# Optimization experiments

Hardware: AMD Instinct MI355X
Metric: run time of the kernel (lower is better)

The kernel has to match this reference:

```python
import jax, jax.numpy as jnp
import numpy as np

NCLASS = 19
BETA = 0.999
IGNORE = -1


def setup_inputs() -> dict:
    key = jax.random.key(0)
    k1, k2 = jax.random.split(key)
    logits = jax.random.normal(k1, (8, NCLASS, 512, 1024), dtype=jnp.float32)
    target = jax.random.randint(k2, (8, 512, 1024), 0, NCLASS, dtype=jnp.int32)
    return {"logits": logits, "target": target}


def _class_balanced_weights(target):
    # Vectorized replacement of the per-sample torch.histc loop.
    B = target.shape[0]
    t = target.reshape(B, -1)
    valid = (t >= 0) & (t < NCLASS)  # histc drops out-of-range (e.g. -1)
    seg = jnp.where(valid, jnp.arange(B, dtype=t.dtype)[:, None] * NCLASS + t, B * NCLASS)
    counts = jax.ops.segment_sum(
        jnp.ones(seg.size, dtype=jnp.float32), seg.reshape(-1),
        num_segments=B * NCLASS + 1)[: B * NCLASS].reshape(B, NCLASS)
    total = counts.sum(axis=0)  # [NCLASS] class counts over whole batch
    w = (1.0 - BETA) / (1.0 - jnp.power(jnp.float32(BETA), total))
    # torch code zeroes the inf entries (classes with zero count)
    return jnp.where(total > 0, w, 0.0)


def reference(logits, target):
    weights = _class_balanced_weights(target)  # [NCLASS]
    logp = jax.nn.log_softmax(logits, axis=1)  # [B, C, H, W]
    tc = jnp.clip(target, 0, NCLASS - 1)
    tgt_logp = jnp.take_along_axis(logp, tc[:, None].astype(jnp.int32), axis=1)[:, 0]  # [B, H, W]
    valid = (target != IGNORE).astype(logits.dtype)
    w_t = weights[tc] * valid  # per-pixel class weight, 0 at ignored pixels
    # PyTorch weighted cross_entropy 'mean': sum(w*nll) / sum(w) over valid
    loss = -(w_t * tgt_logp).sum() / w_t.sum()
    return loss
```

## Files before the change

kernel.cpp:

```cpp
#include <hip/hip_runtime.h>
#include <math.h>

#define NCLASS 19
#define IGNORE_LBL (-1)

constexpr int BDIM   = 8;
constexpr int HWDIM  = 512 * 1024;
constexpr int NPIX   = BDIM * HWDIM;
constexpr int NSTRIP = BDIM * NCLASS;
constexpr int PIXB   = 1024;
constexpr int RING   = 8;
constexpr int DEPTH  = 6;
constexpr double BETA = 0.999;

struct WS {
    double sums[NCLASS];
    int    counts[NCLASS];
};

__global__ void init_ws(WS* ws) {
    int t = threadIdx.x;
    if (t < NCLASS) { ws->sums[t] = 0.0; ws->counts[t] = 0; }
}

typedef const __attribute__((address_space(1))) void* as1_t;
typedef __attribute__((address_space(3))) void*       as3_t;

__device__ __forceinline__ void gload16(const float* g, float* l) {
    __builtin_amdgcn_global_load_lds((as1_t)g, (as3_t)l, 16, 0, 0);
}

__global__ __launch_bounds__(256)
void loss_fused_kernel(const float* __restrict__ logits, const int* __restrict__ tgt,
                       WS* __restrict__ ws) {
    __shared__ __align__(16) float ring[RING][PIXB];
    __shared__ float l_sum[NCLASS];
    __shared__ int   l_cnt[NCLASS];

    const int  tid = threadIdx.x;
    const int  wid = tid >> 6;
    const long px0 = (long)blockIdx.x * PIXB;

    if (tid < NCLASS) { l_sum[tid] = 0.f; l_cnt[tid] = 0; }
    __syncthreads();

    int4 t_cur = *reinterpret_cast<const int4*>(tgt + px0 + 4 * tid);

    const float* gissue = logits + px0 + wid * 256;
    const float* glast  = logits + px0 + (long)(NSTRIP - 1) * HWDIM + wid * 256;

#pragma unroll
    for (int s = 0; s < DEPTH; ++s) {
        gload16(gissue, &ring[s][wid * 256]);
        gissue += HWDIM;
    }

    int slot = 0;

#pragma unroll 1
    for (int b = 0; b < BDIM; ++b) {
        int4 t_nxt = t_cur;
        if (b + 1 < BDIM)
            t_nxt = *reinterpret_cast<const int4*>(
                tgt + (long)(b + 1) * HWDIM + px0 + 4 * tid);

        float s0 = 0.f, s1 = 0.f, s2 = 0.f, s3 = 0.f;
        float ta0 = 0.f, ta1 = 0.f, ta2 = 0.f, ta3 = 0.f;

#pragma unroll
        for (int c = 0; c < NCLASS; ++c) {
            gload16(gissue, &ring[(slot + DEPTH) & (RING - 1)][wid * 256]);
            if (gissue < glast) gissue += HWDIM;
            asm volatile("s_waitcnt vmcnt(6)" ::: "memory");
            __builtin_amdgcn_sched_barrier(0);

            float4 v = *reinterpret_cast<const float4*>(&ring[slot][4 * tid]);
            s0 += __expf(v.x);
            s1 += __expf(v.y);
            s2 += __expf(v.z);
            s3 += __expf(v.w);
            if (c == t_cur.x) ta0 = v.x;
            if (c == t_cur.y) ta1 = v.y;
            if (c == t_cur.z) ta2 = v.z;
            if (c == t_cur.w) ta3 = v.w;
            slot = (slot + 1) & (RING - 1);
        }

        if (t_cur.x >= 0 && t_cur.x < NCLASS) {
            atomicAdd(&l_sum[t_cur.x], ta0 - __logf(s0));
            atomicAdd(&l_cnt[t_cur.x], 1);
        }
        if (t_cur.y >= 0 && t_cur.y < NCLASS) {
            atomicAdd(&l_sum[t_cur.y], ta1 - __logf(s1));
            atomicAdd(&l_cnt[t_cur.y], 1);
        }
        if (t_cur.z >= 0 && t_cur.z < NCLASS) {
            atomicAdd(&l_sum[t_cur.z], ta2 - __logf(s2));
            atomicAdd(&l_cnt[t_cur.z], 1);
        }
        if (t_cur.w >= 0 && t_cur.w < NCLASS) {
            atomicAdd(&l_sum[t_cur.w], ta3 - __logf(s3));
            atomicAdd(&l_cnt[t_cur.w], 1);
        }

        t_cur = t_nxt;
    }

    __syncthreads();
    if (tid < NCLASS) {
        atomicAdd(&ws->sums[tid], (double)l_sum[tid]);
        atomicAdd(&ws->counts[tid], l_cnt[tid]);
    }
}

__global__ void finalize_kernel(const WS* __restrict__ ws, float* __restrict__ out) {
    if (threadIdx.x == 0) {
        double num = 0.0, den = 0.0;
        for (int c = 0; c < NCLASS; ++c) {
            double n = (double)ws->counts[c];
            if (n > 0.0) {
                double w = (1.0 - BETA) / (1.0 - exp(n * log(BETA)));
                num += w * ws->sums[c];
                den += w * n;
            }
        }
        out[0] = (float)(-(num / den));
    }
}

extern "C" void kernel_launch(void* const* d_in, const int* in_sizes, int n_in,
                              void* d_out, int out_size, void* d_ws, size_t ws_size,
                              hipStream_t stream) {
    const float* logits = (const float*)d_in[0];
    const int*   target = (const int*)d_in[1];
    float*       out    = (float*)d_out;
    WS*          ws     = (WS*)d_ws;

    init_ws<<<1, 32, 0, stream>>>(ws);
    loss_fused_kernel<<<HWDIM / PIXB, 256, 0, stream>>>(logits, target, ws);
    finalize_kernel<<<1, 1, 0, stream>>>(ws, out);
}
```

Baseline: 80.29 us.

## Split batch across twice the blocks and replace global atomics with per-block partials

```diff
diff --git a/kernel.cpp b/kernel.cpp
--- a/kernel.cpp
+++ b/kernel.cpp
@@ -6,22 +6,19 @@
 
 constexpr int BDIM   = 8;
 constexpr int HWDIM  = 512 * 1024;
-constexpr int NPIX   = BDIM * HWDIM;
-constexpr int NSTRIP = BDIM * NCLASS;
 constexpr int PIXB   = 1024;
+constexpr int NCOL   = HWDIM / PIXB;
+constexpr int NBLK   = 2 * NCOL;
+constexpr int BPB    = BDIM / 2;
+constexpr int NSTRIP = BPB * NCLASS;
 constexpr int RING   = 8;
 constexpr int DEPTH  = 6;
 constexpr double BETA = 0.999;
 
 struct WS {
-    double sums[NCLASS];
-    int    counts[NCLASS];
+    float psum[NCLASS][NBLK];
+    int   pcnt[NCLASS][NBLK];
 };
-
-__global__ void init_ws(WS* ws) {
-    int t = threadIdx.x;
-    if (t < NCLASS) { ws->sums[t] = 0.0; ws->counts[t] = 0; }
-}
 
 typedef const __attribute__((address_space(1))) void* as1_t;
 typedef __attribute__((address_space(3))) void*       as3_t;
@@ -37,17 +34,21 @@
     __shared__ float l_sum[NCLASS];
     __shared__ int   l_cnt[NCLASS];
 
-    const int  tid = threadIdx.x;
-    const int  wid = tid >> 6;
-    const long px0 = (long)blockIdx.x * PIXB;
+    const int  tid   = threadIdx.x;
+    const int  wid   = tid >> 6;
+    const int  bid   = blockIdx.x;
+    const int  bhalf = bid >> 9;
+    const long px0   = (long)(bid & (NCOL - 1)) * PIXB;
+    const int  img0  = bhalf * BPB;
+    const long pl0   = (long)img0 * NCLASS;
 
     if (tid < NCLASS) { l_sum[tid] = 0.f; l_cnt[tid] = 0; }
     __syncthreads();
 
-    int4 t_cur = *reinterpret_cast<const int4*>(tgt + px0 + 4 * tid);
+    int4 t_cur = *reinterpret_cast<const int4*>(tgt + (long)img0 * HWDIM + px0 + 4 * tid);
 
-    const float* gissue = logits + px0 + wid * 256;
-    const float* glast  = logits + px0 + (long)(NSTRIP - 1) * HWDIM + wid * 256;
+    const float* gissue = logits + pl0 * HWDIM + px0 + wid * 256;
+    const float* glast  = gissue + (long)(NSTRIP - 1) * HWDIM;
 
 #pragma unroll
     for (int s = 0; s < DEPTH; ++s) {
@@ -58,11 +59,11 @@
     int slot = 0;
 
 #pragma unroll 1
-    for (int b = 0; b < BDIM; ++b) {
+    for (int b = 0; b < BPB; ++b) {
         int4 t_nxt = t_cur;
-        if (b + 1 < BDIM)
+        if (b + 1 < BPB)
             t_nxt = *reinterpret_cast<const int4*>(
-                tgt + (long)(b + 1) * HWDIM + px0 + 4 * tid);
+                tgt + (long)(img0 + b + 1) * HWDIM + px0 + 4 * tid);
 
         float s0 = 0.f, s1 = 0.f, s2 = 0.f, s3 = 0.f;
         float ta0 = 0.f, ta1 = 0.f, ta2 = 0.f, ta3 = 0.f;
@@ -108,24 +109,45 @@
 
     __syncthreads();
     if (tid < NCLASS) {
-        atomicAdd(&ws->sums[tid], (double)l_sum[tid]);
-        atomicAdd(&ws->counts[tid], l_cnt[tid]);
+        ws->psum[tid][bid] = l_sum[tid];
+        ws->pcnt[tid][bid] = l_cnt[tid];
     }
 }
 
 __global__ void finalize_kernel(const WS* __restrict__ ws, float* __restrict__ out) {
-    if (threadIdx.x == 0) {
-        double num = 0.0, den = 0.0;
-        for (int c = 0; c < NCLASS; ++c) {
-            double n = (double)ws->counts[c];
-            if (n > 0.0) {
-                double w = (1.0 - BETA) / (1.0 - exp(n * log(BETA)));
-                num += w * ws->sums[c];
-                den += w * n;
+    __shared__ float  sh_s[4];
+    __shared__ int    sh_n[4];
+    __shared__ double sh_num, sh_den;
+
+    const int tid = threadIdx.x, lane = tid & 63, wid = tid >> 6;
+    if (tid == 0) { sh_num = 0.0; sh_den = 0.0; }
+
+    for (int c = 0; c < NCLASS; ++c) {
+        float s = 0.f; int n = 0;
+        for (int i = tid; i < NBLK; i += 256) {
+            s += ws->psum[c][i];
+            n += ws->pcnt[c][i];
+        }
+#pragma unroll
+        for (int off = 32; off > 0; off >>= 1) {
+            s += __shfl_down(s, off);
+            n += __shfl_down(n, off);
+        }
+        __syncthreads();
+        if (lane == 0) { sh_s[wid] = s; sh_n[wid] = n; }
+        __syncthreads();
+        if (tid == 0) {
+            double S = (double)sh_s[0] + sh_s[1] + sh_s[2] + sh_s[3];
+            double N = (double)(sh_n[0] + sh_n[1] + sh_n[2] + sh_n[3]);
+            if (N > 0.0) {
+                double w = (1.0 - BETA) / (1.0 - exp(N * log(BETA)));
+                sh_num += w * S;
+                sh_den += w * N;
             }
         }
-        out[0] = (float)(-(num / den));
     }
+    __syncthreads();
+    if (tid == 0) out[0] = (float)(-(sh_num / sh_den));
 }
 
 extern "C" void kernel_launch(void* const* d_in, const int* in_sizes, int n_in,
@@ -136,7 +158,6 @@
     float*       out    = (float*)d_out;
     WS*          ws     = (WS*)d_ws;
 
-    init_ws<<<1, 32, 0, stream>>>(ws);
-    loss_fused_kernel<<<HWDIM / PIXB, 256, 0, stream>>>(logits, target, ws);
-    finalize_kernel<<<1, 1, 0, stream>>>(ws, out);
+    loss_fused_kernel<<<NBLK, 256, 0, stream>>>(logits, target, ws);
+    finalize_kernel<<<1, 256, 0, stream>>>(ws, out);
 }
```

Measured after the change: 76.95 us. -4.2%, faster.
